# Kernel tuning notes

Hardware: AMD Instinct MI355X
Metric: run time of the kernel (lower is better)

The kernel has to match this reference:

```python
import jax, jax.numpy as jnp
import numpy as np

RATE = 2
KSIZE = 3
STRIDE = 1
SOFTMAX_SCALE = 10.0
EPS_NAN = 1e-4


def resize_bilinear_align(x, oh, ow):
    # torch F.interpolate(mode='bilinear', align_corners=True)
    B, C, H, W = x.shape
    ys = jnp.linspace(0.0, H - 1.0, oh)
    xs = jnp.linspace(0.0, W - 1.0, ow)
    y0 = jnp.floor(ys).astype(jnp.int32)
    y1 = jnp.minimum(y0 + 1, H - 1)
    wy = (ys - y0).astype(x.dtype)
    x0 = jnp.floor(xs).astype(jnp.int32)
    x1 = jnp.minimum(x0 + 1, W - 1)
    wx = (xs - x0).astype(x.dtype)
    t = x[:, :, y0, :] * (1 - wy)[None, None, :, None] + x[:, :, y1, :] * wy[None, None, :, None]
    return t[:, :, :, x0] * (1 - wx) + t[:, :, :, x1] * wx


def extract_patches(x, k, s, pad):
    # x: [C,H,W] -> [L, C, k, k] with SAME padding (pad on each side), L = oh*ow
    C, H, W = x.shape
    xp = jnp.pad(x, ((0, 0), (pad, pad), (pad, pad)))
    oh = (H + 2 * pad - k) // s + 1
    ow = (W + 2 * pad - k) // s + 1
    cols = jnp.stack(
        [xp[:, i:i + s * (oh - 1) + 1:s, j:j + s * (ow - 1) + 1:s]
         for i in range(k) for j in range(k)], axis=0)  # [k*k, C, oh, ow]
    return cols.reshape(k, k, C, oh, ow).transpose(3, 4, 2, 0, 1).reshape(oh * ow, C, k, k)


def conv2d(x, w, padding):
    # x: [N,C,H,W], w: [O,I,kh,kw]
    return jax.lax.conv_general_dilated(
        x, w, (1, 1), [(padding, padding)] * 2,
        dimension_numbers=('NCHW', 'OIHW', 'NCHW'))


def conv_transpose2d(x, w, stride, padding):
    # torch conv_transpose2d: x [N,I,h,w], w [I,O,kh,kw]
    k = w.shape[2]
    wt = jnp.flip(w, (2, 3)).transpose(1, 0, 2, 3)  # [O,I,kh,kw]
    return jax.lax.conv_general_dilated(
        x, wt, (1, 1), [(k - 1 - padding, k - 1 - padding)] * 2,
        lhs_dilation=(stride, stride),
        dimension_numbers=('NCHW', 'OIHW', 'NCHW'))


def setup_inputs() -> dict:
    key = jax.random.key(0)
    k1, k2 = jax.random.split(key)
    B, C, H, W = 4, 64, 128, 128
    background = jax.random.normal(k1, (B, C, H, W), dtype=jnp.float32)
    foreground = jax.random.normal(k2, (B, C, H, W), dtype=jnp.float32)
    return {"background": background, "foreground": foreground}


def reference(background, foreground):
    B, C, H, W = background.shape
    h, w = H // RATE, W // RATE
    fg = resize_bilinear_align(foreground, h, w)  # [B,C,h,w]
    bks = 2 * RATE  # background patch kernel = 4

    def per_sample(fg_i, bg_i):
        # foreground patches [L,C,3,3], L = h*w
        fgp = extract_patches(fg_i, KSIZE, STRIDE, 1)
        norm = jnp.sqrt(jnp.sum(fgp * fgp, axis=(1, 2, 3), keepdims=True))
        fgp_n = fgp / jnp.maximum(norm, EPS_NAN)
        # correlation score [1,L,h,w]
        score = conv2d(fg_i[None], fgp_n, padding=1)
        attn = jax.nn.softmax(score * SOFTMAX_SCALE, axis=1)
        attn = jnp.clip(attn, 1e-8, None)
        # background patches [L,C,4,4] (kernel 4, stride 2, same-pad 1)
        bgp = extract_patches(bg_i, bks, STRIDE * RATE, 1)
        out = conv_transpose2d(attn, bgp, stride=RATE, padding=1) / 4.0
        return out[0]  # [C,H,W]

    return jax.vmap(per_sample)(fg, background)
```

## Files before the change

### kernel.cpp

```cpp
#include <hip/hip_runtime.h>
#include <hip/hip_bf16.h>
#include <math.h>

#define B_  4
#define C_  64
#define H_  128
#define W_  128
#define HS  64
#define WS  64
#define L_  4096
#define K1  576
#define E2  1024
#define ZLOG (-17.5f)

typedef _Float16 f16;
typedef f16 f16x8 __attribute__((ext_vector_type(8)));
typedef float f32x4 __attribute__((ext_vector_type(4)));

__device__ __forceinline__ void gload16(const void* g, void* l) {
    __builtin_amdgcn_global_load_lds(
        (const __attribute__((address_space(1))) unsigned int*)g,
        (__attribute__((address_space(3))) unsigned int*)l, 16, 0, 0);
}

__device__ __forceinline__ int swz(int r, int c) {
    return r * 128 + ((((c >> 3) ^ (r & 7)) << 3) | (c & 7));
}

__global__ __launch_bounds__(256) void resize_kernel(const float* __restrict__ fg,
                                                     float* __restrict__ fgs) {
    int idx = blockIdx.x * 256 + threadIdx.x;
    if (idx >= B_ * C_ * HS * WS) return;
    int j = idx & 63, i = (idx >> 6) & 63, bc = idx >> 12;
    const float sc = 127.0f / 63.0f;
    float yf = i * sc, xf = j * sc;
    int y0 = (int)floorf(yf); if (y0 > 127) y0 = 127;
    int x0 = (int)floorf(xf); if (x0 > 127) x0 = 127;
    int y1 = min(y0 + 1, 127), x1 = min(x0 + 1, 127);
    float wy = yf - (float)y0, wx = xf - (float)x0;
    const float* p = fg + (size_t)bc * (H_ * W_);
    float a = p[y0 * W_ + x0], b = p[y0 * W_ + x1];
    float c = p[y1 * W_ + x0], d = p[y1 * W_ + x1];
    float t0 = a * (1.f - wy) + c * wy;
    float t1 = b * (1.f - wy) + d * wy;
    fgs[idx] = t0 * (1.f - wx) + t1 * wx;
}

__global__ __launch_bounds__(256) void patch_kernel(const float* __restrict__ fgs,
                                                    f16* __restrict__ P_all) {
    int idx = blockIdx.x * 256 + threadIdx.x;
    int b = blockIdx.y;
    int k = idx % K1, l = idx / K1;
    int c = k / 9, r = k % 9;
    int dy = r / 3, dx = r % 3;
    int ly = l >> 6, lx = l & 63;
    int y = ly - 1 + dy, x = lx - 1 + dx;
    float v = 0.f;
    if ((unsigned)y < 64u && (unsigned)x < 64u)
        v = fgs[((size_t)b * C_ + c) * (HS * WS) + y * WS + x];
    P_all[(size_t)b * L_ * K1 + idx] = (f16)v;
}

__global__ __launch_bounds__(64) void norm_kernel(const f16* __restrict__ P_all,
                                                  float* __restrict__ nrm_all) {
    int l = blockIdx.x, b = blockIdx.y, t = threadIdx.x;
    const f16* row = P_all + ((size_t)b * L_ + l) * K1;
    float s = 0.f;
    for (int k = t; k < K1; k += 64) { float v = (float)row[k]; s = fmaf(v, v, s); }
    #pragma unroll
    for (int off = 32; off; off >>= 1) s += __shfl_down(s, off);
    if (t == 0) nrm_all[b * L_ + l] = fmaxf(sqrtf(s), 1e-4f);
}

__global__ __launch_bounds__(256) void v_kernel(const float* __restrict__ bg_b,
                                                f16* __restrict__ VT) {
    int idx = blockIdx.x * 256 + threadIdx.x;
    int l = idx & 4095, e = idx >> 12;
    int c = e >> 4, r = e & 15;
    int ky = r >> 2, kx = r & 3;
    int ly = l >> 6, lx = l & 63;
    int by = 2 * ly - 1 + ky, bx = 2 * lx - 1 + kx;
    float v = 0.f;
    if ((unsigned)by < 128u && (unsigned)bx < 128u)
        v = bg_b[(size_t)c * (H_ * W_) + by * W_ + bx];
    VT[idx] = (f16)v;
}

__device__ __forceinline__ int nextk(int kn, int kLen, unsigned long long mask) {
    while (kn < kLen) {
        int t = kn >> 7;
        if (mask & (1ull << t)) return kn;
        unsigned long long m = mask >> t;
        if (!m) return kLen;
        kn = (t + __builtin_ctzll(m)) << 7;
    }
    return kn;
}

template <int EPI>
__global__ __launch_bounds__(512, 4)
void mfma_gemm(const f16* __restrict__ A, size_t sA,
               const f16* __restrict__ Bt, size_t sB,
               int lda, int ldb, int kLen, void* __restrict__ outp, size_t sOut,
               int ldc, const float* __restrict__ nrm, float* __restrict__ rowsum,
               int* __restrict__ flags) {
    __shared__ __align__(16) f16 As[2][2][128 * 32];
    __shared__ __align__(16) f16 Bs[2][2][128 * 32];
    __shared__ float sred[16];

    const int lin = blockIdx.x;
    const int S = gridDim.x >> 3;
    int bx, by, ls;
    if (EPI == 1) {
        int s = (lin & 7) * S + (lin >> 3);
        int R = s / 136, q = s - R * 136;
        ls = R >> 2;
        int rr = R & 3;
        if (rr < 2) {
            int a = 0;
            while (q >= 16 - a) { q -= 16 - a; ++a; }
            by = a + (rr << 4); bx = a + q + (rr << 4);
        } else {
            if (q >= 128) return;
            by = q & 15; bx = 16 + ((rr & 1) << 3) + (q >> 4);
        }
    } else {
        int G = (lin & 7) * S + (lin >> 3);
        ls = G >> 8;
        by = (G >> 5) & 7; bx = G & 31;
    }

    A  += (size_t)ls * sA;
    Bt += (size_t)ls * sB;
    f16* outbase = (f16*)outp + (size_t)ls * sOut;
    if (EPI == 1) {
        nrm += (size_t)ls * L_; rowsum += (size_t)ls * L_;
        flags += ls * 1024;
    }

    const int tid = threadIdx.x;
    const int w = tid >> 6, lane = tid & 63;
    const int row0 = by * 128, col0 = bx * 128;

    unsigned long long kmask = ~0ull;
    if (EPI == 0) {
        int f = (lane < 32) ? flags[bx * 32 + lane] : 0;
        kmask = __ballot(f != 0);
    }

    const int srow = tid >> 2;
    const int scol = (((tid & 3) ^ ((tid >> 3) & 3)) * 8);
    const f16* gA = A + (size_t)(row0 + srow) * lda + scol;
    const f16* gB = Bt + (size_t)(col0 + srow) * ldb + scol;
    const int ld = tid * 8;

    const int wm = w >> 2, wn = w & 3;
    const int mfm = lane & 15, quad = lane >> 4;
    const int rq = (quad ^ ((mfm >> 1) & 3)) * 8;
    f32x4 acc[4][2] = {};

    int kc = (EPI == 0) ? nextk(0, kLen, kmask) : 0;
    if (kc < kLen) {
        int cur = 0;
        gload16(gA + kc,      &As[0][0][ld]);
        gload16(gA + kc + 32, &As[0][1][ld]);
        gload16(gB + kc,      &Bs[0][0][ld]);
        gload16(gB + kc + 32, &Bs[0][1][ld]);
        for (;;) {
            int kn = (EPI == 0) ? nextk(kc + 64, kLen, kmask) : kc + 64;
            __builtin_amdgcn_s_barrier();
            if (kn < kLen) {
                const int nxt = cur ^ 1;
                gload16(gA + kn,      &As[nxt][0][ld]);
                gload16(gA + kn + 32, &As[nxt][1][ld]);
                gload16(gB + kn,      &Bs[nxt][0][ld]);
                gload16(gB + kn + 32, &Bs[nxt][1][ld]);
                asm volatile("s_waitcnt vmcnt(4)" ::: "memory");
            } else {
                asm volatile("s_waitcnt vmcnt(0)" ::: "memory");
            }
            __builtin_amdgcn_s_barrier();
            __builtin_amdgcn_sched_barrier(0);
            #pragma unroll
            for (int h = 0; h < 2; ++h) {
                f16x8 af[4], bf[2];
                #pragma unroll
                for (int mi = 0; mi < 4; ++mi)
                    af[mi] = *(const f16x8*)&As[cur][h][(wm * 64 + mi * 16 + mfm) * 32 + rq];
                #pragma unroll
                for (int ni = 0; ni < 2; ++ni)
                    bf[ni] = *(const f16x8*)&Bs[cur][h][(wn * 32 + ni * 16 + mfm) * 32 + rq];
                #pragma unroll
                for (int mi = 0; mi < 4; ++mi)
                    #pragma unroll
                    for (int ni = 0; ni < 2; ++ni)
                        acc[mi][ni] = __builtin_amdgcn_mfma_f32_16x16x32_f16(
                            af[mi], bf[ni], acc[mi][ni], 0, 0, 0);
            }
            cur ^= 1;
            kc = kn;
            if (kc >= kLen) break;
        }
    }

    const int orow = row0 + wm * 64;
    const int ocol = col0 + wn * 32;
    f16* st = &As[0][0][0];

    if (EPI == 1) {
        f16* Eo = outbase;
        const bool offd = (by != bx);
        float rowm[16], csr[16], cs[2], cm2[2];
        #pragma unroll
        for (int j = 0; j < 16; ++j) {
            float n = nrm[orow + (j >> 2) * 16 + quad * 4 + (j & 3)];
            rowm[j] = 10.0f * n; csr[j] = 10.0f / n;
        }
        #pragma unroll
        for (int ni = 0; ni < 2; ++ni) {
            float n = nrm[ocol + ni * 16 + mfm];
            cs[ni] = 10.0f / n; cm2[ni] = 10.0f * n;
        }
        float mx1 = -1e30f, mx2 = -1e30f;
        #pragma unroll
        for (int ni = 0; ni < 2; ++ni)
            #pragma unroll
            for (int mi = 0; mi < 4; ++mi)
                #pragma unroll
                for (int r = 0; r < 4; ++r) {
                    float a = acc[mi][ni][r];
                    mx1 = fmaxf(mx1, a * cs[ni] - rowm[mi * 4 + r]);
                    mx2 = fmaxf(mx2, a * csr[mi * 4 + r] - cm2[ni]);
                }
        #pragma unroll
        for (int off = 32; off; off >>= 1) {
            mx1 = fmaxf(mx1, __shfl_xor(mx1, off));
            mx2 = fmaxf(mx2, __shfl_xor(mx2, off));
        }
        if (lane == 0) { sred[w] = mx1; sred[8 + w] = mx2; }
        __syncthreads();
        float b1 = sred[0], b2 = sred[8];
        #pragma unroll
        for (int k = 1; k < 8; ++k) {
            b1 = fmaxf(b1, sred[k]); b2 = fmaxf(b2, sred[8 + k]);
        }
        int nz1 = b1 > ZLOG;
        int nz2 = offd && (b2 > ZLOG);
        if (nz1) {
            float rs[16] = {};
            #pragma unroll
            for (int ni = 0; ni < 2; ++ni)
                #pragma unroll
                for (int mi = 0; mi < 4; ++mi)
                    #pragma unroll
                    for (int r = 0; r < 4; ++r) {
                        float e = __expf(acc[mi][ni][r] * cs[ni] - rowm[mi * 4 + r]);
                        rs[mi * 4 + r] += e;
                        st[swz(wm * 64 + mi * 16 + quad * 4 + r,
                               wn * 32 + ni * 16 + mfm)] = (f16)e;
                    }
            __syncthreads();
            #pragma unroll
            for (int it = 0; it < 4; ++it) {
                int chunk = it * 512 + tid;
                int row = chunk >> 4, c16 = chunk & 15;
                f16x8 v = *(const f16x8*)&st[row * 128 + ((c16 ^ (row & 7)) << 3)];
                *(f16x8*)&Eo[(size_t)(row0 + row) * ldc + col0 + c16 * 8] = v;
            }
            #pragma unroll
            for (int j = 0; j < 16; ++j) {
                float v = rs[j];
                v += __shfl_xor(v, 1); v += __shfl_xor(v, 2);
                v += __shfl_xor(v, 4); v += __shfl_xor(v, 8);
                if (mfm == 0)
                    atomicAdd(&rowsum[orow + (j >> 2) * 16 + quad * 4 + (j & 3)], v);
            }
        }
        if (nz2) {
            __syncthreads();
            float rs2[2] = {};
            #pragma unroll
            for (int ni = 0; ni < 2; ++ni)
                #pragma unroll
                for (int mi = 0; mi < 4; ++mi)
                    #pragma unroll
                    for (int r = 0; r < 4; ++r) {
                        float e = __expf(acc[mi][ni][r] * csr[mi * 4 + r] - cm2[ni]);
                        rs2[ni] += e;
                        st[swz(wn * 32 + ni * 16 + mfm,
                               wm * 64 + mi * 16 + quad * 4 + r)] = (f16)e;
                    }
            __syncthreads();
            #pragma unroll
            for (int it = 0; it < 4; ++it) {
                int chunk = it * 512 + tid;
                int row = chunk >> 4, c16 = chunk & 15;
                f16x8 v = *(const f16x8*)&st[row * 128 + ((c16 ^ (row & 7)) << 3)];
                *(f16x8*)&Eo[(size_t)(col0 + row) * ldc + row0 + c16 * 8] = v;
            }
            #pragma unroll
            for (int ni = 0; ni < 2; ++ni) {
                float v = rs2[ni];
                v += __shfl_xor(v, 16); v += __shfl_xor(v, 32);
                if (quad == 0)
                    atomicAdd(&rowsum[ocol + ni * 16 + mfm], v);
            }
        }
        if (tid == 0) {
            flags[by * 32 + bx] = nz1;
            if (offd) flags[bx * 32 + by] = nz2;
        }
    } else {
        __syncthreads();
        #pragma unroll
        for (int ni = 0; ni < 2; ++ni)
            #pragma unroll
            for (int mi = 0; mi < 4; ++mi)
                #pragma unroll
                for (int r = 0; r < 4; ++r)
                    st[swz(wm * 64 + mi * 16 + quad * 4 + r,
                           wn * 32 + ni * 16 + mfm)] = (f16)acc[mi][ni][r];
        __syncthreads();
        f16* base = outbase + (size_t)row0 * ldc + col0;
        #pragma unroll
        for (int it = 0; it < 4; ++it) {
            int chunk = it * 512 + tid;
            int row = chunk >> 4, c16 = chunk & 15;
            f16x8 v = *(const f16x8*)&st[row * 128 + ((c16 ^ (row & 7)) << 3)];
            *(f16x8*)&base[(size_t)row * ldc + c16 * 8] = v;
        }
    }
}

__global__ __launch_bounds__(256) void gather_kernel(const f16* __restrict__ OPT,
                                                     const float* __restrict__ rowsum,
                                                     float* __restrict__ out_b) {
    int idx = blockIdx.x * 256 + threadIdx.x;
    if (idx >= C_ * H_ * W_) return;
    int X = idx & 127, Y = (idx >> 7) & 127, c = idx >> 14;
    int kyp = (Y + 1) & 1;
    int kxp = (X + 1) & 1;
    float sum = 0.f;
    #pragma unroll
    for (int ky = kyp; ky < 4; ky += 2) {
        int py = (Y + 1 - ky) >> 1;
        if ((unsigned)py >= 64u) continue;
        #pragma unroll
        for (int kx = kxp; kx < 4; kx += 2) {
            int px = (X + 1 - kx) >> 1;
            if ((unsigned)px >= 64u) continue;
            int p = py * 64 + px;
            int e = c * 16 + ky * 4 + kx;
            float v = (float)OPT[(size_t)e * L_ + p];
            sum += v * __builtin_amdgcn_rcpf(rowsum[p]);
        }
    }
    out_b[idx] = 0.25f * sum;
}

extern "C" void kernel_launch(void* const* d_in, const int* in_sizes, int n_in,
                              void* d_out, int out_size, void* d_ws, size_t ws_size,
                              hipStream_t stream) {
    const float* bg = (const float*)d_in[0];
    const float* fg = (const float*)d_in[1];
    float* out = (float*)d_out;
    char* w8 = (char*)d_ws;

    float* fgs        = (float*)(w8);
    f16*   P_all      = (f16*)  (w8 + 4194304);
    float* nrm        = (float*)(w8 + 23068672);
    float* rowsum_all = (float*)(w8 + 23134208);
    int*   flags      = (int*)  (w8 + 23199744);
    const size_t base = 23216128;

    const size_t EB_ELEMS = (size_t)L_ * L_;
    f16* Eb_all = (f16*)(w8 + base);
    f16* VT     = (f16*)(w8 + base + 4 * EB_ELEMS * 2);
    f16* OPT    = (f16*)(w8 + base + 4 * EB_ELEMS * 2 + (size_t)E2 * L_ * 2);

    resize_kernel<<<(B_ * C_ * HS * WS) / 256, 256, 0, stream>>>(fg, fgs);
    patch_kernel<<<dim3((L_ * K1) / 256, B_), 256, 0, stream>>>(fgs, P_all);
    norm_kernel<<<dim3(L_, B_), 64, 0, stream>>>(P_all, nrm);
    hipMemsetAsync(rowsum_all, 0, (size_t)B_ * L_ * sizeof(float), stream);

    mfma_gemm<1><<<2176, 512, 0, stream>>>(
        P_all, (size_t)L_ * K1, P_all, (size_t)L_ * K1,
        K1, K1, K1, Eb_all, EB_ELEMS, L_,
        nrm, rowsum_all, flags);

    for (int b = 0; b < B_; ++b) {
        const f16* Eb_b    = Eb_all + (size_t)b * EB_ELEMS;
        const float* rs_b  = rowsum_all + (size_t)b * L_;
        int* flags_b       = flags + b * 1024;

        v_kernel<<<(L_ * E2) / 256, 256, 0, stream>>>(
            bg + (size_t)b * C_ * H_ * W_, VT);

        mfma_gemm<0><<<256, 512, 0, stream>>>(
            VT, 0, Eb_b, 0,
            L_, L_, L_, OPT, 0, L_,
            nullptr, nullptr, flags_b);

        gather_kernel<<<(C_ * H_ * W_) / 256, 256, 0, stream>>>(
            OPT, rs_b, out + (size_t)b * C_ * H_ * W_);
    }
}
```

Before: 266.1 us.

## Fuse gather into GEMM epilogue with atomics, batch PV GEMM, fold norm into patches

The col2im gather and the 1/rowsum scaling now run inside the second GEMM's epilogue. Each tile scatters its scaled fp32 results straight into the zeroed output with atomicAdd, so the f16 OPT intermediate and the gather kernel are gone. The v_kernel and the PV GEMM now cover several batches per launch (all four if the workspace is large enough), cutting per-batch launches. The separate norm kernel is replaced by wave reductions plus atomics in the patch kernel, and the sqrt and clamp move into the first GEMM's epilogue. In exchange the code takes on many global float atomics, whose summation order is not fixed, so results can vary slightly from run to run.

Result: slower. 342.2 us (+28.6%).

```diff
diff --git a/kernel.cpp b/kernel.cpp
--- a/kernel.cpp
+++ b/kernel.cpp
@@ -47,7 +47,8 @@
 }
 
 __global__ __launch_bounds__(256) void patch_kernel(const float* __restrict__ fgs,
-                                                    f16* __restrict__ P_all) {
+                                                    f16* __restrict__ P_all,
+                                                    float* __restrict__ nrmsq) {
     int idx = blockIdx.x * 256 + threadIdx.x;
     int b = blockIdx.y;
     int k = idx % K1, l = idx / K1;
@@ -59,21 +60,17 @@
     if ((unsigned)y < 64u && (unsigned)x < 64u)
         v = fgs[((size_t)b * C_ + c) * (HS * WS) + y * WS + x];
     P_all[(size_t)b * L_ * K1 + idx] = (f16)v;
-}
-
-__global__ __launch_bounds__(64) void norm_kernel(const f16* __restrict__ P_all,
-                                                  float* __restrict__ nrm_all) {
-    int l = blockIdx.x, b = blockIdx.y, t = threadIdx.x;
-    const f16* row = P_all + ((size_t)b * L_ + l) * K1;
-    float s = 0.f;
-    for (int k = t; k < K1; k += 64) { float v = (float)row[k]; s = fmaf(v, v, s); }
+    float s = v * v;
     #pragma unroll
     for (int off = 32; off; off >>= 1) s += __shfl_down(s, off);
-    if (t == 0) nrm_all[b * L_ + l] = fmaxf(sqrtf(s), 1e-4f);
-}
-
-__global__ __launch_bounds__(256) void v_kernel(const float* __restrict__ bg_b,
-                                                f16* __restrict__ VT) {
+    if ((threadIdx.x & 63) == 0) atomicAdd(&nrmsq[b * L_ + l], s);
+}
+
+__global__ __launch_bounds__(256) void v_kernel(const float* __restrict__ bg_g,
+                                                f16* __restrict__ VT_g) {
+    int ls = blockIdx.y;
+    const float* bg_b = bg_g + (size_t)ls * (C_ * H_ * W_);
+    f16* VT = VT_g + (size_t)ls * ((size_t)E2 * L_);
     int idx = blockIdx.x * 256 + threadIdx.x;
     int l = idx & 4095, e = idx >> 12;
     int c = e >> 4, r = e & 15;
@@ -132,11 +129,9 @@
 
     A  += (size_t)ls * sA;
     Bt += (size_t)ls * sB;
-    f16* outbase = (f16*)outp + (size_t)ls * sOut;
-    if (EPI == 1) {
-        nrm += (size_t)ls * L_; rowsum += (size_t)ls * L_;
-        flags += ls * 1024;
-    }
+    rowsum += (size_t)ls * L_;
+    flags  += ls * 1024;
+    if (EPI == 1) nrm += (size_t)ls * L_;
 
     const int tid = threadIdx.x;
     const int w = tid >> 6, lane = tid & 63;
@@ -205,20 +200,20 @@
 
     const int orow = row0 + wm * 64;
     const int ocol = col0 + wn * 32;
-    f16* st = &As[0][0][0];
 
     if (EPI == 1) {
-        f16* Eo = outbase;
+        f16* st = &As[0][0][0];
+        f16* Eo = (f16*)outp + (size_t)ls * sOut;
         const bool offd = (by != bx);
         float rowm[16], csr[16], cs[2], cm2[2];
         #pragma unroll
         for (int j = 0; j < 16; ++j) {
-            float n = nrm[orow + (j >> 2) * 16 + quad * 4 + (j & 3)];
+            float n = fmaxf(sqrtf(nrm[orow + (j >> 2) * 16 + quad * 4 + (j & 3)]), 1e-4f);
             rowm[j] = 10.0f * n; csr[j] = 10.0f / n;
         }
         #pragma unroll
         for (int ni = 0; ni < 2; ++ni) {
-            float n = nrm[ocol + ni * 16 + mfm];
+            float n = fmaxf(sqrtf(nrm[ocol + ni * 16 + mfm]), 1e-4f);
             cs[ni] = 10.0f / n; cm2[ni] = 10.0f * n;
         }
         float mx1 = -1e30f, mx2 = -1e30f;
@@ -311,51 +306,28 @@
             if (offd) flags[bx * 32 + by] = nz2;
         }
     } else {
-        __syncthreads();
+        float* Oo = (float*)outp + (size_t)ls * sOut;
+        float rcpRS[2];
         #pragma unroll
         for (int ni = 0; ni < 2; ++ni)
-            #pragma unroll
-            for (int mi = 0; mi < 4; ++mi)
-                #pragma unroll
-                for (int r = 0; r < 4; ++r)
-                    st[swz(wm * 64 + mi * 16 + quad * 4 + r,
-                           wn * 32 + ni * 16 + mfm)] = (f16)acc[mi][ni][r];
-        __syncthreads();
-        f16* base = outbase + (size_t)row0 * ldc + col0;
-        #pragma unroll
-        for (int it = 0; it < 4; ++it) {
-            int chunk = it * 512 + tid;
-            int row = chunk >> 4, c16 = chunk & 15;
-            f16x8 v = *(const f16x8*)&st[row * 128 + ((c16 ^ (row & 7)) << 3)];
-            *(f16x8*)&base[(size_t)row * ldc + c16 * 8] = v;
-        }
-    }
-}
-
-__global__ __launch_bounds__(256) void gather_kernel(const f16* __restrict__ OPT,
-                                                     const float* __restrict__ rowsum,
-                                                     float* __restrict__ out_b) {
-    int idx = blockIdx.x * 256 + threadIdx.x;
-    if (idx >= C_ * H_ * W_) return;
-    int X = idx & 127, Y = (idx >> 7) & 127, c = idx >> 14;
-    int kyp = (Y + 1) & 1;
-    int kxp = (X + 1) & 1;
-    float sum = 0.f;
-    #pragma unroll
-    for (int ky = kyp; ky < 4; ky += 2) {
-        int py = (Y + 1 - ky) >> 1;
-        if ((unsigned)py >= 64u) continue;
-        #pragma unroll
-        for (int kx = kxp; kx < 4; kx += 2) {
-            int px = (X + 1 - kx) >> 1;
-            if ((unsigned)px >= 64u) continue;
-            int p = py * 64 + px;
-            int e = c * 16 + ky * 4 + kx;
-            float v = (float)OPT[(size_t)e * L_ + p];
-            sum += v * __builtin_amdgcn_rcpf(rowsum[p]);
-        }
-    }
-    out_b[idx] = 0.25f * sum;
+            rcpRS[ni] = 0.25f * __builtin_amdgcn_rcpf(rowsum[ocol + ni * 16 + mfm]);
+        #pragma unroll
+        for (int mi = 0; mi < 4; ++mi)
+            #pragma unroll
+            for (int r = 0; r < 4; ++r) {
+                int e = orow + mi * 16 + quad * 4 + r;
+                int c = e >> 4, ky = (e >> 2) & 3, kx = e & 3;
+                #pragma unroll
+                for (int ni = 0; ni < 2; ++ni) {
+                    int p = ocol + ni * 16 + mfm;
+                    int Y = 2 * (p >> 6) - 1 + ky;
+                    int X = 2 * (p & 63) - 1 + kx;
+                    if ((unsigned)Y < 128u && (unsigned)X < 128u)
+                        atomicAdd(&Oo[((size_t)c << 14) + (Y << 7) + X],
+                                  acc[mi][ni][r] * rcpRS[ni]);
+                }
+            }
+    }
 }
 
 extern "C" void kernel_launch(void* const* d_in, const int* in_sizes, int n_in,
@@ -368,40 +340,35 @@
 
     float* fgs        = (float*)(w8);
     f16*   P_all      = (f16*)  (w8 + 4194304);
-    float* nrm        = (float*)(w8 + 23068672);
+    float* nrmsq      = (float*)(w8 + 23068672);
     float* rowsum_all = (float*)(w8 + 23134208);
     int*   flags      = (int*)  (w8 + 23199744);
     const size_t base = 23216128;
 
     const size_t EB_ELEMS = (size_t)L_ * L_;
+    const size_t VT_BYTES = (size_t)E2 * L_ * 2;
     f16* Eb_all = (f16*)(w8 + base);
-    f16* VT     = (f16*)(w8 + base + 4 * EB_ELEMS * 2);
-    f16* OPT    = (f16*)(w8 + base + 4 * EB_ELEMS * 2 + (size_t)E2 * L_ * 2);
+    f16* VT_all = (f16*)(w8 + base + 4 * EB_ELEMS * 2);
+    int nbb = (ws_size >= base + 4 * EB_ELEMS * 2 + 4 * VT_BYTES) ? 4 : 2;
+
+    hipMemsetAsync(nrmsq, 0, 131072, stream);
+    hipMemsetAsync(out, 0, (size_t)B_ * C_ * H_ * W_ * sizeof(float), stream);
 
     resize_kernel<<<(B_ * C_ * HS * WS) / 256, 256, 0, stream>>>(fg, fgs);
-    patch_kernel<<<dim3((L_ * K1) / 256, B_), 256, 0, stream>>>(fgs, P_all);
-    norm_kernel<<<dim3(L_, B_), 64, 0, stream>>>(P_all, nrm);
-    hipMemsetAsync(rowsum_all, 0, (size_t)B_ * L_ * sizeof(float), stream);
+    patch_kernel<<<dim3((L_ * K1) / 256, B_), 256, 0, stream>>>(fgs, P_all, nrmsq);
 
     mfma_gemm<1><<<2176, 512, 0, stream>>>(
         P_all, (size_t)L_ * K1, P_all, (size_t)L_ * K1,
         K1, K1, K1, Eb_all, EB_ELEMS, L_,
-        nrm, rowsum_all, flags);
-
-    for (int b = 0; b < B_; ++b) {
-        const f16* Eb_b    = Eb_all + (size_t)b * EB_ELEMS;
-        const float* rs_b  = rowsum_all + (size_t)b * L_;
-        int* flags_b       = flags + b * 1024;
-
-        v_kernel<<<(L_ * E2) / 256, 256, 0, stream>>>(
-            bg + (size_t)b * C_ * H_ * W_, VT);
-
-        mfma_gemm<0><<<256, 512, 0, stream>>>(
-            VT, 0, Eb_b, 0,
-            L_, L_, L_, OPT, 0, L_,
-            nullptr, nullptr, flags_b);
-
-        gather_kernel<<<(C_ * H_ * W_) / 256, 256, 0, stream>>>(
-            OPT, rs_b, out + (size_t)b * C_ * H_ * W_);
-    }
-}
+        nrmsq, rowsum_all, flags);
+
+    for (int g = 0; g < B_; g += nbb) {
+        v_kernel<<<dim3((L_ * E2) / 256, nbb), 256, 0, stream>>>(
+            bg + (size_t)g * C_ * H_ * W_, VT_all);
+
+        mfma_gemm<0><<<256 * nbb, 512, 0, stream>>>(
+            VT_all, (size_t)E2 * L_, Eb_all + (size_t)g * EB_ELEMS, EB_ELEMS,
+            L_, L_, L_, out + (size_t)g * C_ * H_ * W_, (size_t)C_ * H_ * W_, 0,
+            nullptr, rowsum_all + (size_t)g * L_, flags + g * 1024);
+    }
+}
```

## Fuse patch norm into patch kernel and batch attention GEMM over sample pairs

Applied to the files above, without the earlier changes.

Removes the separate norm kernel. Each wave in the patch kernel now reduces its squared values and atomically adds them into a per-row squared-norm buffer, and the score GEMM epilogue takes the sqrt and clamp. The per-sample loop of v_kernel, GEMM and gather now handles two samples per launch using grid.y and batch strides. This doubles the GEMM grid to fill more CUs and halves the launch count. OPT now reuses the freed front of the workspace, and a single memset clears both the norm and rowsum buffers. The trade-offs are float atomics, which make the sum order nondeterministic, and a larger VT/OPT footprint.

After: 249.1 us. 1.07x faster.

```diff
diff --git a/kernel.cpp b/kernel.cpp
--- a/kernel.cpp
+++ b/kernel.cpp
@@ -47,7 +47,8 @@
 }
 
 __global__ __launch_bounds__(256) void patch_kernel(const float* __restrict__ fgs,
-                                                    f16* __restrict__ P_all) {
+                                                    f16* __restrict__ P_all,
+                                                    float* __restrict__ nrmsq) {
     int idx = blockIdx.x * 256 + threadIdx.x;
     int b = blockIdx.y;
     int k = idx % K1, l = idx / K1;
@@ -59,21 +60,17 @@
     if ((unsigned)y < 64u && (unsigned)x < 64u)
         v = fgs[((size_t)b * C_ + c) * (HS * WS) + y * WS + x];
     P_all[(size_t)b * L_ * K1 + idx] = (f16)v;
-}
-
-__global__ __launch_bounds__(64) void norm_kernel(const f16* __restrict__ P_all,
-                                                  float* __restrict__ nrm_all) {
-    int l = blockIdx.x, b = blockIdx.y, t = threadIdx.x;
-    const f16* row = P_all + ((size_t)b * L_ + l) * K1;
-    float s = 0.f;
-    for (int k = t; k < K1; k += 64) { float v = (float)row[k]; s = fmaf(v, v, s); }
+    float s = v * v;
     #pragma unroll
     for (int off = 32; off; off >>= 1) s += __shfl_down(s, off);
-    if (t == 0) nrm_all[b * L_ + l] = fmaxf(sqrtf(s), 1e-4f);
-}
-
-__global__ __launch_bounds__(256) void v_kernel(const float* __restrict__ bg_b,
-                                                f16* __restrict__ VT) {
+    if ((threadIdx.x & 63) == 0) atomicAdd(&nrmsq[b * L_ + l], s);
+}
+
+__global__ __launch_bounds__(256) void v_kernel(const float* __restrict__ bg_g,
+                                                f16* __restrict__ VT_g) {
+    int ls = blockIdx.y;
+    const float* bg_b = bg_g + (size_t)ls * (C_ * H_ * W_);
+    f16* VT = VT_g + (size_t)ls * ((size_t)E2 * L_);
     int idx = blockIdx.x * 256 + threadIdx.x;
     int l = idx & 4095, e = idx >> 12;
     int c = e >> 4, r = e & 15;
@@ -133,10 +130,8 @@
     A  += (size_t)ls * sA;
     Bt += (size_t)ls * sB;
     f16* outbase = (f16*)outp + (size_t)ls * sOut;
-    if (EPI == 1) {
-        nrm += (size_t)ls * L_; rowsum += (size_t)ls * L_;
-        flags += ls * 1024;
-    }
+    if (EPI == 1) { nrm += (size_t)ls * L_; rowsum += (size_t)ls * L_; }
+    flags += ls * 1024;
 
     const int tid = threadIdx.x;
     const int w = tid >> 6, lane = tid & 63;
@@ -213,12 +208,12 @@
         float rowm[16], csr[16], cs[2], cm2[2];
         #pragma unroll
         for (int j = 0; j < 16; ++j) {
-            float n = nrm[orow + (j >> 2) * 16 + quad * 4 + (j & 3)];
+            float n = fmaxf(sqrtf(nrm[orow + (j >> 2) * 16 + quad * 4 + (j & 3)]), 1e-4f);
             rowm[j] = 10.0f * n; csr[j] = 10.0f / n;
         }
         #pragma unroll
         for (int ni = 0; ni < 2; ++ni) {
-            float n = nrm[ocol + ni * 16 + mfm];
+            float n = fmaxf(sqrtf(nrm[ocol + ni * 16 + mfm]), 1e-4f);
             cs[ni] = 10.0f / n; cm2[ni] = 10.0f * n;
         }
         float mx1 = -1e30f, mx2 = -1e30f;
@@ -332,9 +327,13 @@
     }
 }
 
-__global__ __launch_bounds__(256) void gather_kernel(const f16* __restrict__ OPT,
-                                                     const float* __restrict__ rowsum,
-                                                     float* __restrict__ out_b) {
+__global__ __launch_bounds__(256) void gather_kernel(const f16* __restrict__ OPT_g,
+                                                     const float* __restrict__ rowsum_g,
+                                                     float* __restrict__ out_g) {
+    int ls = blockIdx.y;
+    const f16* OPT = OPT_g + (size_t)ls * ((size_t)E2 * L_);
+    const float* rowsum = rowsum_g + (size_t)ls * L_;
+    float* out_b = out_g + (size_t)ls * (C_ * H_ * W_);
     int idx = blockIdx.x * 256 + threadIdx.x;
     if (idx >= C_ * H_ * W_) return;
     int X = idx & 127, Y = (idx >> 7) & 127, c = idx >> 14;
@@ -368,40 +367,36 @@
 
     float* fgs        = (float*)(w8);
     f16*   P_all      = (f16*)  (w8 + 4194304);
-    float* nrm        = (float*)(w8 + 23068672);
+    float* nrmsq      = (float*)(w8 + 23068672);
     float* rowsum_all = (float*)(w8 + 23134208);
     int*   flags      = (int*)  (w8 + 23199744);
     const size_t base = 23216128;
 
     const size_t EB_ELEMS = (size_t)L_ * L_;
-    f16* Eb_all = (f16*)(w8 + base);
-    f16* VT     = (f16*)(w8 + base + 4 * EB_ELEMS * 2);
-    f16* OPT    = (f16*)(w8 + base + 4 * EB_ELEMS * 2 + (size_t)E2 * L_ * 2);
+    f16* Eb_all  = (f16*)(w8 + base);
+    f16* VT_all  = (f16*)(w8 + base + 4 * EB_ELEMS * 2);
+    f16* OPT_all = (f16*)w8;
+
+    hipMemsetAsync(nrmsq, 0, 131072, stream);
 
     resize_kernel<<<(B_ * C_ * HS * WS) / 256, 256, 0, stream>>>(fg, fgs);
-    patch_kernel<<<dim3((L_ * K1) / 256, B_), 256, 0, stream>>>(fgs, P_all);
-    norm_kernel<<<dim3(L_, B_), 64, 0, stream>>>(P_all, nrm);
-    hipMemsetAsync(rowsum_all, 0, (size_t)B_ * L_ * sizeof(float), stream);
+    patch_kernel<<<dim3((L_ * K1) / 256, B_), 256, 0, stream>>>(fgs, P_all, nrmsq);
 
     mfma_gemm<1><<<2176, 512, 0, stream>>>(
         P_all, (size_t)L_ * K1, P_all, (size_t)L_ * K1,
         K1, K1, K1, Eb_all, EB_ELEMS, L_,
-        nrm, rowsum_all, flags);
-
-    for (int b = 0; b < B_; ++b) {
-        const f16* Eb_b    = Eb_all + (size_t)b * EB_ELEMS;
-        const float* rs_b  = rowsum_all + (size_t)b * L_;
-        int* flags_b       = flags + b * 1024;
-
-        v_kernel<<<(L_ * E2) / 256, 256, 0, stream>>>(
-            bg + (size_t)b * C_ * H_ * W_, VT);
-
-        mfma_gemm<0><<<256, 512, 0, stream>>>(
-            VT, 0, Eb_b, 0,
-            L_, L_, L_, OPT, 0, L_,
-            nullptr, nullptr, flags_b);
-
-        gather_kernel<<<(C_ * H_ * W_) / 256, 256, 0, stream>>>(
-            OPT, rs_b, out + (size_t)b * C_ * H_ * W_);
-    }
-}
+        nrmsq, rowsum_all, flags);
+
+    for (int g = 0; g < B_; g += 2) {
+        v_kernel<<<dim3((L_ * E2) / 256, 2), 256, 0, stream>>>(
+            bg + (size_t)g * C_ * H_ * W_, VT_all);
+
+        mfma_gemm<0><<<512, 512, 0, stream>>>(
+            VT_all, (size_t)E2 * L_, Eb_all + (size_t)g * EB_ELEMS, EB_ELEMS,
+            L_, L_, L_, OPT_all, (size_t)E2 * L_, L_,
+            nullptr, nullptr, flags + g * 1024);
+
+        gather_kernel<<<dim3((C_ * H_ * W_) / 256, 2), 256, 0, stream>>>(
+            OPT_all, rowsum_all + (size_t)g * L_, out + (size_t)g * C_ * H_ * W_);
+    }
+}
```
